# Kernel optimization log

Measured on AMD Instinct MI355X. Metric: run time of the kernel, lower is better.

The kernel has to match this reference:

```python
import jax, jax.numpy as jnp
import numpy as np

NUM_EXPERTS = 8
TOP_K = 2
HIDDEN = 2048
INTER = 768


def setup_inputs() -> dict:
    key = jax.random.key(0)
    k0, k1, k2, k3, k4 = jax.random.split(key, 5)
    return {
        "hidden_states": jax.random.normal(k0, (2, 1024, HIDDEN), jnp.float32),
        "gate_w": jax.random.normal(k1, (NUM_EXPERTS, HIDDEN), jnp.float32) * 0.02,
        "w_gate": jax.random.normal(k2, (NUM_EXPERTS, HIDDEN, INTER), jnp.float32) * 0.02,
        "w_up": jax.random.normal(k3, (NUM_EXPERTS, HIDDEN, INTER), jnp.float32) * 0.02,
        "w_down": jax.random.normal(k4, (NUM_EXPERTS, INTER, HIDDEN), jnp.float32) * 0.02,
    }


def reference(hidden_states, gate_w, w_gate, w_up, w_down):
    B, S, H = hidden_states.shape
    x = hidden_states.reshape(-1, H)            # [T, H]
    T = x.shape[0]

    # Router: softmax in fp32, top-k, renormalize (norm_topk_prob=True)
    router_logits = jnp.einsum('td,ed->te', x, gate_w)          # [T, E]
    probs = jax.nn.softmax(router_logits.astype(jnp.float32), axis=-1)
    top_w, top_i = jax.lax.top_k(probs, TOP_K)                  # [T, K]
    top_w = top_w / jnp.sum(top_w, axis=-1, keepdims=True)
    top_w = top_w.astype(x.dtype)

    # Dense combine weights [T, E]: zero for unselected experts.
    # (top-k indices are distinct per token, so .set is exact.)
    w_dense = jnp.zeros((T, NUM_EXPERTS), x.dtype).at[
        jnp.arange(T)[:, None], top_i].set(top_w)

    # Per-expert SwiGLU MLP (Qwen3MoeMLP): down(silu(gate(x)) * up(x)).
    # EP dispatch/combine with ep_size=1 is an identity permutation, so the
    # math equals running every selected (token, expert) pair and combining.
    g = jax.nn.silu(jnp.einsum('td,edf->etf', x, w_gate))       # [E, T, F]
    u = jnp.einsum('td,edf->etf', x, w_up)                      # [E, T, F]
    y = jnp.einsum('etf,efd->etd', g * u, w_down)               # [E, T, H]

    out = jnp.einsum('etd,te->td', y, w_dense)                  # [T, H]
    return out.reshape(B, S, H), router_logits
```

## Files before the change

### kernel.cpp

```cpp
#include <hip/hip_runtime.h>
#include <hip/hip_bf16.h>
#include <math.h>

#define NTOK 2048
#define HID 2048
#define NEXP 8
#define FINT 768
#define TOPK 2

typedef __attribute__((ext_vector_type(8))) short bf16x8;
typedef __attribute__((ext_vector_type(4))) float f32x4;

static __device__ __forceinline__ unsigned short f2bf(float f) {
    union { float f; unsigned u; } v; v.f = f;
    unsigned r = v.u + 0x7fffu + ((v.u >> 16) & 1u);
    return (unsigned short)(r >> 16);
}

static __device__ __forceinline__ void gl16(const void* g, void* l) {
    __builtin_amdgcn_global_load_lds(
        (const __attribute__((address_space(1))) unsigned int*)g,
        (__attribute__((address_space(3))) unsigned int*)(uintptr_t)l,
        16, 0, 0);
}


static __device__ __forceinline__ void transpose_tile(
        const float* __restrict__ src, unsigned short* __restrict__ dst,
        int R, int C, int r0, int c0, float* tile, int tid) {
    {
        int rbase = tid >> 4;
        int ch = tid & 15;
        #pragma unroll
        for (int i = 0; i < 4; ++i) {
            int row = i * 16 + rbase;
            float4 v = *(const float4*)&src[(size_t)(r0 + row) * C + c0 + ch * 4];
            int p = ch ^ (row & 15);
            *(float4*)&tile[row * 64 + p * 4] = v;
        }
    }
    __syncthreads();
    {
        int r16 = (tid & 15) * 4;
        int cg = tid >> 4;
        float4 v[4];
        #pragma unroll
        for (int j = 0; j < 4; ++j) {
            int row = r16 + j;
            int p = cg ^ (row & 15);
            v[j] = *(const float4*)&tile[row * 64 + p * 4];
        }
        #pragma unroll
        for (int i = 0; i < 4; ++i) {
            float c0v = (i == 0) ? v[0].x : (i == 1) ? v[0].y : (i == 2) ? v[0].z : v[0].w;
            float c1v = (i == 0) ? v[1].x : (i == 1) ? v[1].y : (i == 2) ? v[1].z : v[1].w;
            float c2v = (i == 0) ? v[2].x : (i == 1) ? v[2].y : (i == 2) ? v[2].z : v[2].w;
            float c3v = (i == 0) ? v[3].x : (i == 1) ? v[3].y : (i == 2) ? v[3].z : v[3].w;
            ushort4 o = make_ushort4(f2bf(c0v), f2bf(c1v), f2bf(c2v), f2bf(c3v));
            *(uint2*)&dst[(size_t)(c0 + cg * 4 + i) * R + r0 + r16] = *(const uint2*)&o;
        }
    }
}

__global__ __launch_bounds__(256) void k1_all(
        const float* __restrict__ x,
        const float* __restrict__ gw,
        const float* __restrict__ wg, const float* __restrict__ wu,
        const float* __restrict__ wd,
        float* __restrict__ out,
        float* __restrict__ logits_out,
        int* __restrict__ topk_idx,
        float* __restrict__ topk_w,
        unsigned short* __restrict__ xb,
        unsigned short* __restrict__ wgt, unsigned short* __restrict__ wut,
        unsigned short* __restrict__ wdt) {
    __shared__ __align__(16) float tile[64 * 64];
    int bid = blockIdx.x;
    if (bid < 512) {
        int w = threadIdx.x >> 6, l = threadIdx.x & 63;
        int t = bid * 4 + w;
        const float4* xr = (const float4*)(x + (size_t)t * HID);
        unsigned short* xbr = xb + (size_t)t * HID;
        float4 v[8];
        #pragma unroll
        for (int i = 0; i < 8; ++i) v[i] = xr[i * 64 + l];
        #pragma unroll
        for (int i = 0; i < 8; ++i)
            *(ushort4*)&xbr[(i * 64 + l) * 4] =
                make_ushort4(f2bf(v[i].x), f2bf(v[i].y), f2bf(v[i].z), f2bf(v[i].w));
        {
            float4 z = make_float4(0.f, 0.f, 0.f, 0.f);
            float4* orow = (float4*)(out + (size_t)t * HID);
            #pragma unroll
            for (int i = 0; i < 8; ++i) orow[i * 64 + l] = z;
        }
        float acc[NEXP];
        #pragma unroll
        for (int e = 0; e < NEXP; ++e) {
            const float4* gr = (const float4*)(gw + (size_t)e * HID);
            float a = 0.f;
            #pragma unroll
            for (int i = 0; i < 8; ++i) {
                float4 g = gr[i * 64 + l];
                a += v[i].x * g.x + v[i].y * g.y + v[i].z * g.z + v[i].w * g.w;
            }
            acc[e] = a;
        }
        #pragma unroll
        for (int off = 32; off > 0; off >>= 1)
            #pragma unroll
            for (int e = 0; e < NEXP; ++e) acc[e] += __shfl_xor(acc[e], off);
        if (l == 0) {
            float m = -1e30f;
            #pragma unroll
            for (int i = 0; i < NEXP; ++i) m = fmaxf(m, acc[i]);
            float p[NEXP];
            #pragma unroll
            for (int i = 0; i < NEXP; ++i) p[i] = expf(acc[i] - m);
            int i0 = 0;
            #pragma unroll
            for (int i = 1; i < NEXP; ++i) if (p[i] > p[i0]) i0 = i;
            int i1 = (i0 == 0) ? 1 : 0;
            #pragma unroll
            for (int i = 0; i < NEXP; ++i) if (i != i0 && p[i] > p[i1]) i1 = i;
            float w0 = p[i0], w1 = p[i1], sw = w0 + w1;
            topk_idx[t * 2 + 0] = i0;
            topk_idx[t * 2 + 1] = i1;
            topk_w[t * 2 + 0] = w0 / sw;
            topk_w[t * 2 + 1] = w1 / sw;
            #pragma unroll
            for (int i = 0; i < NEXP; ++i) logits_out[(size_t)t * NEXP + i] = acc[i];
        }
    } else if (bid < 6656) {
        int idx = bid - 512;
        int e = idx / 768, sub = idx % 768;
        const float* src; unsigned short* dst;
        if (sub < 384) { src = wg; dst = wgt; }
        else           { src = wu; dst = wut; sub -= 384; }
        int tr = sub / 12, tc = sub % 12;
        src += (size_t)e * HID * FINT;
        dst += (size_t)e * HID * FINT;
        transpose_tile(src, dst, HID, FINT, tr * 64, tc * 64, tile, threadIdx.x);
    } else {
        int idx = bid - 6656;
        int e = idx / 384, sub = idx % 384;
        int tr = sub / 32, tc = sub % 32;
        transpose_tile(wd + (size_t)e * FINT * HID,
                       wdt + (size_t)e * FINT * HID,
                       FINT, HID, tr * 64, tc * 64, tile, threadIdx.x);
    }
}

__global__ void moe_build_kernel(const int* __restrict__ topk_idx,
                                 const float* __restrict__ topk_w,
                                 int* __restrict__ counts,
                                 int* __restrict__ offsets,
                                 int* __restrict__ elist_t,
                                 float* __restrict__ elist_w,
                                 int* __restrict__ row_token,
                                 float* __restrict__ row_w) {
    __shared__ int scnt[NEXP];
    __shared__ int soff[NEXP];
    int tid = threadIdx.x;
    if (tid < NEXP) scnt[tid] = 0;
    __syncthreads();
    for (int t = tid; t < NTOK; t += 1024) {
        #pragma unroll
        for (int k = 0; k < TOPK; ++k) {
            int e = topk_idx[t * 2 + k];
            float w = topk_w[t * 2 + k];
            int slot = atomicAdd(&scnt[e], 1);
            elist_t[e * NTOK + slot] = t;
            elist_w[e * NTOK + slot] = w;
        }
    }
    __syncthreads();
    if (tid == 0) {
        int o = 0;
        for (int e = 0; e < NEXP; ++e) {
            soff[e] = o; offsets[e] = o; counts[e] = scnt[e]; o += scnt[e];
        }
    }
    __syncthreads();
    for (int e = 0; e < NEXP; ++e) {
        int c = scnt[e], o = soff[e];
        for (int s = tid; s < c; s += 1024) {
            row_token[o + s] = elist_t[e * NTOK + s];
            row_w[o + s]     = elist_w[e * NTOK + s];
        }
    }
}

__global__ __launch_bounds__(256) void moe_stage_a_mfma(
        const unsigned short* __restrict__ xb,
        const unsigned short* __restrict__ wgt,
        const unsigned short* __restrict__ wut,
        const int* __restrict__ counts,
        const int* __restrict__ offsets,
        const int* __restrict__ row_token,
        unsigned short* __restrict__ h_buf) {
    int e = blockIdx.x, mt = blockIdx.y, nt = blockIdx.z;
    int count = counts[e];
    int m0 = mt * 64;
    if (m0 >= count) return;
    int off = offsets[e];
    int n0 = nt * 64;
    int mcnt = min(64, count - m0);
    int tid = threadIdx.x;

    __shared__ __align__(16) unsigned short As[2][64 * 64];
    __shared__ __align__(16) unsigned short Bg[2][64 * 64];
    __shared__ __align__(16) unsigned short Bu[2][64 * 64];
    __shared__ int toks[64];
    if (tid < 64) toks[tid] = row_token[off + m0 + min(tid, mcnt - 1)];
    __syncthreads();

    int w = tid >> 6, l = tid & 63;
    int wr = w >> 1, wc = w & 1;
    int lr = l & 15, lh = l >> 4;
    int rA = w * 8 + (l >> 3);
    int cA = l & 7;

    const unsigned short* wgE = wgt + (size_t)e * FINT * HID + (size_t)n0 * HID;
    const unsigned short* wuE = wut + (size_t)e * FINT * HID + (size_t)n0 * HID;

    f32x4 gacc[2][2] = {};
    f32x4 uacc[2][2] = {};

    auto STAGE = [&](int buf, int k0) {
        #pragma unroll
        for (int i = 0; i < 2; ++i) {
            int row = 32 * i + rA;
            int sc = (cA ^ (row & 7)) << 3;
            size_t db = (size_t)(32 * i + w * 8) * 128;
            gl16(xb + (size_t)toks[row] * HID + k0 + sc, (char*)&As[buf][0] + db);
            gl16(wgE + (size_t)row * HID + k0 + sc,      (char*)&Bg[buf][0] + db);
            gl16(wuE + (size_t)row * HID + k0 + sc,      (char*)&Bu[buf][0] + db);
        }
    };

    auto COMPUTE = [&](int buf) {
        #pragma unroll
        for (int ks = 0; ks < 2; ++ks) {
            bf16x8 af[2], bg[2], bu[2];
            #pragma unroll
            for (int mi = 0; mi < 2; ++mi) {
                int row = wr * 32 + mi * 16 + lr;
                int byte = row * 128 + ((ks * 64 + lh * 16) ^ ((row & 7) << 4));
                af[mi] = *(const bf16x8*)((const char*)&As[buf][0] + byte);
            }
            #pragma unroll
            for (int ni = 0; ni < 2; ++ni) {
                int row = wc * 32 + ni * 16 + lr;
                int byte = row * 128 + ((ks * 64 + lh * 16) ^ ((row & 7) << 4));
                bg[ni] = *(const bf16x8*)((const char*)&Bg[buf][0] + byte);
                bu[ni] = *(const bf16x8*)((const char*)&Bu[buf][0] + byte);
            }
            #pragma unroll
            for (int mi = 0; mi < 2; ++mi)
                #pragma unroll
                for (int ni = 0; ni < 2; ++ni) {
                    gacc[mi][ni] = __builtin_amdgcn_mfma_f32_16x16x32_bf16(af[mi], bg[ni], gacc[mi][ni], 0, 0, 0);
                    uacc[mi][ni] = __builtin_amdgcn_mfma_f32_16x16x32_bf16(af[mi], bu[ni], uacc[mi][ni], 0, 0, 0);
                }
        }
    };

    STAGE(0, 0);
    __syncthreads();
    for (int t = 0; t < HID / 64; ++t) {
        int cur = t & 1;
        if (t + 1 < HID / 64) STAGE(cur ^ 1, (t + 1) * 64);
        COMPUTE(cur);
        __syncthreads();
    }

    #pragma unroll
    for (int mi = 0; mi < 2; ++mi)
        #pragma unroll
        for (int ni = 0; ni < 2; ++ni)
            #pragma unroll
            for (int j = 0; j < 4; ++j) {
                int row = wr * 32 + mi * 16 + lh * 4 + j;
                if (row < mcnt) {
                    int col = wc * 32 + ni * 16 + lr;
                    float g = gacc[mi][ni][j], u = uacc[mi][ni][j];
                    float hv = g / (1.f + expf(-g)) * u;
                    h_buf[(size_t)(off + m0 + row) * FINT + n0 + col] = f2bf(hv);
                }
            }
}

__global__ __launch_bounds__(256) void moe_stage_b_mfma(
        const unsigned short* __restrict__ h_buf,
        const unsigned short* __restrict__ wdt,
        const int* __restrict__ counts,
        const int* __restrict__ offsets,
        const int* __restrict__ row_token,
        const float* __restrict__ row_w,
        float* __restrict__ out) {
    int e = blockIdx.x, mt = blockIdx.y, nt = blockIdx.z;
    int count = counts[e];
    int m0 = mt * 128;
    if (m0 >= count) return;
    int off = offsets[e];
    int n0 = nt * 128;
    int mcnt = min(128, count - m0);
    int tid = threadIdx.x;

    __shared__ __align__(16) unsigned short As[2][128 * 64];
    __shared__ __align__(16) unsigned short Bs[2][128 * 64];
    __shared__ int toks[128];
    __shared__ float rws[128];
    if (tid < 128) {
        int mm = min(tid, mcnt - 1);
        toks[tid] = row_token[off + m0 + mm];
        rws[tid] = row_w[off + m0 + mm];
    }
    __syncthreads();

    int w = tid >> 6, l = tid & 63;
    int wr = w >> 1, wc = w & 1;
    int lr = l & 15, lh = l >> 4;
    int wbase = (tid & 192) * 16;

    const unsigned short* hb = h_buf + (size_t)(off + m0) * FINT;
    const unsigned short* wdE = wdt + (size_t)e * HID * FINT + (size_t)n0 * FINT;

    f32x4 acc[4][4] = {};

    auto STAGE = [&](int buf, int k0) {
        #pragma unroll
        for (int i = 0; i < 4; ++i) {
            int s = i * 256 + tid;
            int row = s >> 3, c = s & 7;
            int sc = (c ^ (row & 7)) << 3;
            gl16(hb + (size_t)row * FINT + k0 + sc,  (char*)&As[buf][0] + i * 4096 + wbase);
            gl16(wdE + (size_t)row * FINT + k0 + sc, (char*)&Bs[buf][0] + i * 4096 + wbase);
        }
    };

    auto COMPUTE = [&](int buf) {
        #pragma unroll
        for (int ks = 0; ks < 2; ++ks) {
            bf16x8 af[4], bf[4];
            #pragma unroll
            for (int mi = 0; mi < 4; ++mi) {
                int row = wr * 64 + mi * 16 + lr;
                int byte = row * 128 + ((ks * 64 + lh * 16) ^ ((row & 7) << 4));
                af[mi] = *(const bf16x8*)((const char*)&As[buf][0] + byte);
            }
            #pragma unroll
            for (int ni = 0; ni < 4; ++ni) {
                int row = wc * 64 + ni * 16 + lr;
                int byte = row * 128 + ((ks * 64 + lh * 16) ^ ((row & 7) << 4));
                bf[ni] = *(const bf16x8*)((const char*)&Bs[buf][0] + byte);
            }
            #pragma unroll
            for (int mi = 0; mi < 4; ++mi)
                #pragma unroll
                for (int ni = 0; ni < 4; ++ni)
                    acc[mi][ni] = __builtin_amdgcn_mfma_f32_16x16x32_bf16(af[mi], bf[ni], acc[mi][ni], 0, 0, 0);
        }
    };

    STAGE(0, 0);
    __syncthreads();
    for (int t = 0; t < FINT / 64; ++t) {
        int cur = t & 1;
        if (t + 1 < FINT / 64) STAGE(cur ^ 1, (t + 1) * 64);
        COMPUTE(cur);
        __syncthreads();
    }

    #pragma unroll
    for (int mi = 0; mi < 4; ++mi)
        #pragma unroll
        for (int ni = 0; ni < 4; ++ni)
            #pragma unroll
            for (int j = 0; j < 4; ++j) {
                int row = wr * 64 + mi * 16 + lh * 4 + j;
                if (row < mcnt) {
                    int col = n0 + wc * 64 + ni * 16 + lr;
                    atomicAdd(&out[(size_t)toks[row] * HID + col],
                              rws[row] * acc[mi][ni][j]);
                }
            }
}

extern "C" void kernel_launch(void* const* d_in, const int* in_sizes, int n_in,
                              void* d_out, int out_size, void* d_ws, size_t ws_size,
                              hipStream_t stream) {
    const float* x       = (const float*)d_in[0];
    const float* gate_w  = (const float*)d_in[1];
    const float* w_gate  = (const float*)d_in[2];
    const float* w_up    = (const float*)d_in[3];
    const float* w_down  = (const float*)d_in[4];
    float* out = (float*)d_out;

    char* ws = (char*)d_ws;
    int*   topk_idx  = (int*)  (ws + 0);
    float* topk_w    = (float*)(ws + 16384);
    int*   counts    = (int*)  (ws + 32768);
    int*   offsets   = (int*)  (ws + 32800);
    int*   row_token = (int*)  (ws + 33024);
    float* row_w     = (float*)(ws + 49408);
    int*   elist_t   = (int*)  (ws + 65792);
    float* elist_w   = (float*)(ws + 131328);

    unsigned short* xb   = (unsigned short*)(ws + 196864);
    unsigned short* wg_t = (unsigned short*)(ws + 8585472);
    unsigned short* wu_t = (unsigned short*)(ws + 33751296);
    unsigned short* wd_t = (unsigned short*)(ws + 58917120);
    unsigned short* hb   = (unsigned short*)(ws + 84082944);

    float* logits_out = out + (size_t)NTOK * HID;

    k1_all<<<9728, 256, 0, stream>>>(
        x, gate_w, w_gate, w_up, w_down, out, logits_out,
        topk_idx, topk_w, xb, wg_t, wu_t, wd_t);
    moe_build_kernel<<<1, 1024, 0, stream>>>(topk_idx, topk_w, counts, offsets,
                                             elist_t, elist_w, row_token, row_w);
    dim3 gridA(NEXP, NTOK / 64, FINT / 64);
    moe_stage_a_mfma<<<gridA, 256, 0, stream>>>(xb, wg_t, wu_t, counts, offsets,
                                                row_token, hb);
    dim3 gridB(NEXP, NTOK / 128, HID / 128);
    moe_stage_b_mfma<<<gridB, 256, 0, stream>>>(hb, wd_t, counts, offsets,
                                                row_token, row_w, out);
}
```

Before: 149.3 us.

## Process four transpose tiles per block with double-buffered LDS prefetch

```diff
diff --git a/kernel.cpp b/kernel.cpp
--- a/kernel.cpp
+++ b/kernel.cpp
@@ -25,41 +25,28 @@
 }
 
 
-static __device__ __forceinline__ void transpose_tile(
-        const float* __restrict__ src, unsigned short* __restrict__ dst,
-        int R, int C, int r0, int c0, float* tile, int tid) {
-    {
-        int rbase = tid >> 4;
-        int ch = tid & 15;
-        #pragma unroll
-        for (int i = 0; i < 4; ++i) {
-            int row = i * 16 + rbase;
-            float4 v = *(const float4*)&src[(size_t)(r0 + row) * C + c0 + ch * 4];
-            int p = ch ^ (row & 15);
-            *(float4*)&tile[row * 64 + p * 4] = v;
-        }
-    }
-    __syncthreads();
-    {
-        int r16 = (tid & 15) * 4;
-        int cg = tid >> 4;
-        float4 v[4];
-        #pragma unroll
-        for (int j = 0; j < 4; ++j) {
-            int row = r16 + j;
-            int p = cg ^ (row & 15);
-            v[j] = *(const float4*)&tile[row * 64 + p * 4];
-        }
-        #pragma unroll
-        for (int i = 0; i < 4; ++i) {
-            float c0v = (i == 0) ? v[0].x : (i == 1) ? v[0].y : (i == 2) ? v[0].z : v[0].w;
-            float c1v = (i == 0) ? v[1].x : (i == 1) ? v[1].y : (i == 2) ? v[1].z : v[1].w;
-            float c2v = (i == 0) ? v[2].x : (i == 1) ? v[2].y : (i == 2) ? v[2].z : v[2].w;
-            float c3v = (i == 0) ? v[3].x : (i == 1) ? v[3].y : (i == 2) ? v[3].z : v[3].w;
-            ushort4 o = make_ushort4(f2bf(c0v), f2bf(c1v), f2bf(c2v), f2bf(c3v));
-            *(uint2*)&dst[(size_t)(c0 + cg * 4 + i) * R + r0 + r16] = *(const uint2*)&o;
-        }
-    }
+struct TP { const float* s; unsigned short* d; int R, C, r0, c0; };
+
+static __device__ __forceinline__ TP tp_decode(
+        int t,
+        const float* wg, const float* wu, const float* wd,
+        unsigned short* wgt, unsigned short* wut, unsigned short* wdt) {
+    TP p;
+    if (t < 6144) {
+        int e = t / 768, sub = t % 768;
+        if (sub < 384) { p.s = wg; p.d = wgt; }
+        else           { p.s = wu; p.d = wut; sub -= 384; }
+        p.R = HID; p.C = FINT;
+        p.r0 = (sub / 12) * 64; p.c0 = (sub % 12) * 64;
+        p.s += (size_t)e * HID * FINT; p.d += (size_t)e * HID * FINT;
+    } else {
+        t -= 6144;
+        int e = t / 384, sub = t % 384;
+        p.s = wd + (size_t)e * FINT * HID; p.d = wdt + (size_t)e * FINT * HID;
+        p.R = FINT; p.C = HID;
+        p.r0 = (sub / 32) * 64; p.c0 = (sub % 32) * 64;
+    }
+    return p;
 }
 
 __global__ __launch_bounds__(256) void k1_all(
@@ -74,7 +61,7 @@
         unsigned short* __restrict__ xb,
         unsigned short* __restrict__ wgt, unsigned short* __restrict__ wut,
         unsigned short* __restrict__ wdt) {
-    __shared__ __align__(16) float tile[64 * 64];
+    __shared__ __align__(16) float tile2[2][64 * 64];
     int bid = blockIdx.x;
     if (bid < 512) {
         int w = threadIdx.x >> 6, l = threadIdx.x & 63;
@@ -131,23 +118,59 @@
             #pragma unroll
             for (int i = 0; i < NEXP; ++i) logits_out[(size_t)t * NEXP + i] = acc[i];
         }
-    } else if (bid < 6656) {
-        int idx = bid - 512;
-        int e = idx / 768, sub = idx % 768;
-        const float* src; unsigned short* dst;
-        if (sub < 384) { src = wg; dst = wgt; }
-        else           { src = wu; dst = wut; sub -= 384; }
-        int tr = sub / 12, tc = sub % 12;
-        src += (size_t)e * HID * FINT;
-        dst += (size_t)e * HID * FINT;
-        transpose_tile(src, dst, HID, FINT, tr * 64, tc * 64, tile, threadIdx.x);
     } else {
-        int idx = bid - 6656;
-        int e = idx / 384, sub = idx % 384;
-        int tr = sub / 32, tc = sub % 32;
-        transpose_tile(wd + (size_t)e * FINT * HID,
-                       wdt + (size_t)e * FINT * HID,
-                       FINT, HID, tr * 64, tc * 64, tile, threadIdx.x);
+        int g = (bid - 512) * 4;
+        int tid = threadIdx.x;
+        int rbase = tid >> 4, ch = tid & 15;
+        int pswz = (ch ^ rbase) * 4;
+        int r16 = (tid & 15) * 4, cg = tid >> 4;
+
+        TP cur = tp_decode(g, wg, wu, wd, wgt, wut, wdt);
+        float4 ld[4];
+        #pragma unroll
+        for (int i = 0; i < 4; ++i)
+            ld[i] = *(const float4*)&cur.s[(size_t)(cur.r0 + i * 16 + rbase) * cur.C
+                                           + cur.c0 + ch * 4];
+        #pragma unroll
+        for (int i = 0; i < 4; ++i)
+            *(float4*)&tile2[0][(i * 16 + rbase) * 64 + pswz] = ld[i];
+        __syncthreads();
+
+        for (int it = 0; it < 4; ++it) {
+            int cb = it & 1;
+            TP nxt;
+            if (it < 3) {
+                nxt = tp_decode(g + it + 1, wg, wu, wd, wgt, wut, wdt);
+                #pragma unroll
+                for (int i = 0; i < 4; ++i)
+                    ld[i] = *(const float4*)&nxt.s[(size_t)(nxt.r0 + i * 16 + rbase) * nxt.C
+                                                   + nxt.c0 + ch * 4];
+            }
+            float4 v[4];
+            #pragma unroll
+            for (int j = 0; j < 4; ++j) {
+                int row = r16 + j;
+                int p = cg ^ (row & 15);
+                v[j] = *(const float4*)&tile2[cb][row * 64 + p * 4];
+            }
+            #pragma unroll
+            for (int i2 = 0; i2 < 4; ++i2) {
+                float c0v = (i2 == 0) ? v[0].x : (i2 == 1) ? v[0].y : (i2 == 2) ? v[0].z : v[0].w;
+                float c1v = (i2 == 0) ? v[1].x : (i2 == 1) ? v[1].y : (i2 == 2) ? v[1].z : v[1].w;
+                float c2v = (i2 == 0) ? v[2].x : (i2 == 1) ? v[2].y : (i2 == 2) ? v[2].z : v[2].w;
+                float c3v = (i2 == 0) ? v[3].x : (i2 == 1) ? v[3].y : (i2 == 2) ? v[3].z : v[3].w;
+                ushort4 o = make_ushort4(f2bf(c0v), f2bf(c1v), f2bf(c2v), f2bf(c3v));
+                *(uint2*)&cur.d[(size_t)(cur.c0 + cg * 4 + i2) * cur.R + cur.r0 + r16] =
+                    *(const uint2*)&o;
+            }
+            if (it < 3) {
+                #pragma unroll
+                for (int i = 0; i < 4; ++i)
+                    *(float4*)&tile2[cb ^ 1][(i * 16 + rbase) * 64 + pswz] = ld[i];
+                cur = nxt;
+            }
+            __syncthreads();
+        }
     }
 }
 
@@ -416,7 +439,7 @@
 
     float* logits_out = out + (size_t)NTOK * HID;
 
-    k1_all<<<9728, 256, 0, stream>>>(
+    k1_all<<<512 + 2304, 256, 0, stream>>>(
         x, gate_w, w_gate, w_up, w_down, out, logits_out,
         topk_idx, topk_w, xb, wg_t, wu_t, wd_t);
     moe_build_kernel<<<1, 1024, 0, stream>>>(topk_idx, topk_w, counts, offsets,
```

Result: slower. 177.1 us (+18.6%).
